# Performance work log

Hardware: AMD Instinct MI355X
Metric: run time of the kernel (lower is better)

The kernel has to match this reference:

```python
import jax, jax.numpy as jnp
import numpy as np

DIM = 1024
N_HEADS = 16
HEAD_DIM = DIM // N_HEADS
BATCH = 2
SEQ = 2048


def rotate_half(x):
    x1, x2 = jnp.split(x, 2, axis=-1)
    return jnp.concatenate((-x2, x1), axis=-1)


def rope_cos_sin(seq_len, head_dim, dtype=jnp.float32):
    inv_freq = 1.0 / (10000.0 ** (jnp.arange(0, head_dim, 2, dtype=jnp.float32) / head_dim))
    t = jnp.arange(seq_len, dtype=jnp.float32)
    freqs = jnp.einsum('i,j->ij', t, inv_freq)          # [S, hd/2]
    emb = jnp.concatenate((freqs, freqs), axis=-1)       # [S, hd]
    return emb.astype(dtype)[None, :, None, :]           # [1, S, 1, hd] (cos/sin applied below)


def setup_inputs() -> dict:
    key = jax.random.key(0)
    k_x, k_q, k_k, k_v, k_o = jax.random.split(key, 5)
    scale = 1.0 / np.sqrt(DIM)
    x = jax.random.normal(k_x, (BATCH, SEQ, DIM), dtype=jnp.float32)
    Wq = jax.random.normal(k_q, (DIM, DIM), dtype=jnp.float32) * scale
    Wk = jax.random.normal(k_k, (DIM, DIM), dtype=jnp.float32) * scale
    Wv = jax.random.normal(k_v, (DIM, DIM), dtype=jnp.float32) * scale
    Wo = jax.random.normal(k_o, (DIM, DIM), dtype=jnp.float32) * scale
    # causal mask: scores masked where mask == 0
    mask = jnp.tril(jnp.ones((SEQ, SEQ), dtype=jnp.int32))[None, None, :, :]
    return {"x": x, "Wq": Wq, "Wk": Wk, "Wv": Wv, "Wo": Wo, "mask": mask}


def reference(x, Wq, Wk, Wv, Wo, mask):
    B, S, _ = x.shape
    # torch nn.Linear: y = x @ W.T
    q = (x @ Wq.T).reshape(B, S, N_HEADS, HEAD_DIM)
    k = (x @ Wk.T).reshape(B, S, N_HEADS, HEAD_DIM)
    v = (x @ Wv.T).reshape(B, S, N_HEADS, HEAD_DIM)
    ang = rope_cos_sin(S, HEAD_DIM, x.dtype)
    cos, sin = jnp.cos(ang), jnp.sin(ang)
    q = q * cos + rotate_half(q) * sin
    k = k * cos + rotate_half(k) * sin
    # [B, H, S, hd]
    q = q.transpose(0, 2, 1, 3)
    k = k.transpose(0, 2, 1, 3)
    v = v.transpose(0, 2, 1, 3)
    scores = jnp.einsum('bhqd,bhkd->bhqk', q, k) / np.sqrt(HEAD_DIM)
    scores = jnp.where(mask == 0, jnp.asarray(-1e9, scores.dtype), scores)
    attn = jax.nn.softmax(scores, axis=-1)
    out = jnp.einsum('bhqk,bhkd->bhqd', attn, v)
    out = out.transpose(0, 2, 1, 3).reshape(B, S, DIM)
    return out @ Wo.T
```

## Files before the change

kernel.cpp:

```cpp
#include <hip/hip_runtime.h>
#include <stdint.h>

typedef unsigned short u16;
typedef __bf16 bf16x8 __attribute__((ext_vector_type(8)));
typedef __bf16 bf16x4 __attribute__((ext_vector_type(4)));
typedef float f32x4 __attribute__((ext_vector_type(4)));

#define N_B 2
#define N_S 2048
#define N_D 1024
#define N_H 16
#define HD 64

#if __has_builtin(__builtin_amdgcn_exp2f)
#define EXP2F(x) __builtin_amdgcn_exp2f(x)
#else
#define EXP2F(x) exp2f(x)
#endif

__device__ __forceinline__ u16 f2bf(float f) {
  union { float f; uint32_t u; } v; v.f = f;
  uint32_t u = v.u + 0x7fffu + ((v.u >> 16) & 1u);
  return (u16)(u >> 16);
}

__device__ __forceinline__ void gload16(const u16* g, u16* lds) {
  __builtin_amdgcn_global_load_lds(
      (const __attribute__((address_space(1))) unsigned int*)g,
      (__attribute__((address_space(3))) unsigned int*)lds, 16, 0, 0);
}

__global__ __launch_bounds__(256) void prep_kernel(
    const float* __restrict__ x, const float* __restrict__ Wq,
    const float* __restrict__ Wk, const float* __restrict__ Wv,
    const float* __restrict__ Wo,
    u16* __restrict__ xb, u16* __restrict__ wqb, u16* __restrict__ wkb,
    u16* __restrict__ wvb, u16* __restrict__ wob,
    float* __restrict__ cosT, float* __restrict__ sinT)
{
  const int NX = N_B * N_S * N_D;
  const int NW = N_D * N_D;
  int bid = blockIdx.x;
  if (bid < 8192) {
    int i = (bid * 256 + threadIdx.x) * 4;
    const float* src; u16* dst; int off;
    if (i < NX) { src = x; dst = xb; off = i; }
    else {
      int j = i - NX;
      int w = j >> 20;
      off = j & (NW - 1);
      src = (w == 0) ? Wq : (w == 1) ? Wk : (w == 2) ? Wv : Wo;
      dst = (w == 0) ? wqb : (w == 1) ? wkb : (w == 2) ? wvb : wob;
    }
    float4 v = *(const float4*)(src + off);
    ushort4 o;
    o.x = f2bf(v.x); o.y = f2bf(v.y); o.z = f2bf(v.z); o.w = f2bf(v.w);
    *(ushort4*)(dst + off) = o;
  } else {
    int t = (bid - 8192) * 256 + threadIdx.x;
    int s = t >> 5, i = t & 31;
    float inv = expf(-(float)i * 0.28782313662425574f);
    float a = (float)s * inv;
    float sn, cs;
    sincosf(a, &sn, &cs);
    cosT[t] = cs;
    sinT[t] = sn;
  }
}

__global__ __launch_bounds__(256, 5) void proj_kernel(
    const u16* __restrict__ x, const u16* __restrict__ Wq,
    const u16* __restrict__ Wk, const u16* __restrict__ Wv,
    u16* __restrict__ Qb, u16* __restrict__ Kb, u16* __restrict__ Vtb,
    const float* __restrict__ cosT, const float* __restrict__ sinT)
{
  const int mode = blockIdx.z;
  const u16* Wm = (mode == 0) ? Wq : (mode == 1) ? Wk : Wv;
  const int bx = blockIdx.x, by = blockIdx.y;
  const int tid = threadIdx.x;
  const int wave = tid >> 6, lane = tid & 63;
  const int c = lane & 15, quad = lane >> 4;

  __shared__ __align__(16) u16 As[128 * 64];
  __shared__ __align__(16) u16 Bs[64 * 64];

  const f32x4 zero = {0.f, 0.f, 0.f, 0.f};
  f32x4 acc[2][4];
#pragma unroll
  for (int i = 0; i < 2; ++i)
#pragma unroll
    for (int j = 0; j < 4; ++j) acc[i][j] = zero;

  for (int kt = 0; kt < 16; ++kt) {
    const int k0 = kt * 64;
    __syncthreads();
#pragma unroll
    for (int t = 0; t < 4; ++t) {
      int p = t * 256 + tid;
      int m = p >> 3, sl = p & 7;
      int kq = sl ^ (m & 7);
      gload16(x + (size_t)(by * 128 + m) * N_D + k0 + kq * 8, &As[(t * 256 + wave * 64) * 8]);
    }
#pragma unroll
    for (int t = 0; t < 2; ++t) {
      int p = t * 256 + tid;
      int m = p >> 3, sl = p & 7;
      int kq = sl ^ (m & 7);
      gload16(Wm + (size_t)(bx * 64 + m) * N_D + k0 + kq * 8, &Bs[(t * 256 + wave * 64) * 8]);
    }
    __syncthreads();
#pragma unroll
    for (int ks = 0; ks < 2; ++ks) {
      bf16x8 av[2], bv[4];
      int kq = ks * 4 + quad;
#pragma unroll
      for (int i = 0; i < 2; ++i) {
        int m = wave * 32 + i * 16 + c;
        av[i] = *(const bf16x8*)&As[(m * 8 + (kq ^ (m & 7))) * 8];
      }
#pragma unroll
      for (int j = 0; j < 4; ++j) {
        int n = j * 16 + c;
        bv[j] = *(const bf16x8*)&Bs[(n * 8 + (kq ^ (n & 7))) * 8];
      }
#pragma unroll
      for (int i = 0; i < 2; ++i)
#pragma unroll
        for (int j = 0; j < 4; ++j)
          acc[i][j] = __builtin_amdgcn_mfma_f32_16x16x32_bf16(av[i], bv[j], acc[i][j], 0, 0, 0);
    }
  }

  const int h = bx;
  if (mode < 2) {
    u16* Out = (mode == 0) ? Qb : Kb;
#pragma unroll
    for (int i = 0; i < 2; ++i) {
#pragma unroll
      for (int r = 0; r < 4; ++r) {
        int row = by * 128 + wave * 32 + i * 16 + quad * 4 + r;
        int b = row >> 11, s = row & 2047;
        float cs0 = cosT[s * 32 + c],      sn0 = sinT[s * 32 + c];
        float cs1 = cosT[s * 32 + 16 + c], sn1 = sinT[s * 32 + 16 + c];
        size_t base = ((size_t)(b * N_H + h) * N_S + s) * HD;
#pragma unroll
        for (int j = 0; j < 4; ++j) {
          float v = acc[i][j][r];
          float p = acc[i][j ^ 2][r];
          float cs = (j & 1) ? cs1 : cs0;
          float sn = (j & 1) ? sn1 : sn0;
          float res = (j < 2) ? (v * cs - p * sn) : (v * cs + p * sn);
          Out[base + j * 16 + c] = f2bf(res);
        }
      }
    }
  } else {
#pragma unroll
    for (int i = 0; i < 2; ++i) {
      int srow = by * 128 + wave * 32 + i * 16 + quad * 4;
      int b = srow >> 11, sb = srow & 2047;
#pragma unroll
      for (int j = 0; j < 4; ++j) {
        int d = j * 16 + c;
        ushort4 pk;
        pk.x = f2bf(acc[i][j][0]);
        pk.y = f2bf(acc[i][j][1]);
        pk.z = f2bf(acc[i][j][2]);
        pk.w = f2bf(acc[i][j][3]);
        *(ushort4*)&Vtb[((size_t)(b * N_H + h) * HD + d) * N_S + sb] = pk;
      }
    }
  }
}

__global__ __launch_bounds__(64, 2) void attn_kernel(
    const u16* __restrict__ Qb, const u16* __restrict__ Kb,
    const u16* __restrict__ Vtb, u16* __restrict__ Ab)
{
  const int lane = threadIdx.x;
  const int c = lane & 15, quad = lane >> 4;
  const int bx = blockIdx.x;
  const int xcd = bx & 7;
  const int idx = bx >> 3;
  const int t = 63 - (idx >> 2);
  const int bh = xcd + (idx & 3) * 8;
  const int q0 = t * 32;
  const int ktmax = t >> 1;
  const int maskch = t & 1;

  __shared__ __align__(16) u16 Ks[2][64 * 64];
  __shared__ __align__(16) u16 Ps[32 * 32];

  const u16* Qg = Qb + ((size_t)bh * N_S + q0) * HD;
  const u16* Kg = Kb + (size_t)bh * N_S * HD;
  const u16* Vg = Vtb + (size_t)bh * HD * N_S;

  bf16x8 qreg[2][2];
#pragma unroll
  for (int jQ = 0; jQ < 2; ++jQ)
#pragma unroll
    for (int ks = 0; ks < 2; ++ks)
      qreg[jQ][ks] = *(const bf16x8*)(Qg + (jQ * 16 + c) * HD + ks * 32 + quad * 8);

  const f32x4 zero = {0.f, 0.f, 0.f, 0.f};
  f32x4 acc_o[2][4];
#pragma unroll
  for (int mt = 0; mt < 2; ++mt)
#pragma unroll
    for (int nt = 0; nt < 4; ++nt) acc_o[mt][nt] = zero;
  float lrow[2] = {0.f, 0.f};

  const float CLOG = 0.18033688011112042f;
  const float FM = 16.0f;

#pragma unroll
  for (int i = 0; i < 8; ++i) {
    int ci = i * 64 + lane;
    int m = ci >> 3, sl = ci & 7;
    int kq = sl ^ (m & 7);
    gload16(Kg + (size_t)m * HD + kq * 8, &Ks[0][i * 512]);
  }
  asm volatile("" ::: "memory");
  bf16x8 vf[2][4];
#pragma unroll
  for (int ch = 0; ch < 2; ++ch)
#pragma unroll
    for (int nt = 0; nt < 4; ++nt)
      vf[ch][nt] = *(const bf16x8*)(Vg + (size_t)(nt * 16 + c) * N_S + ch * 32 + quad * 8);

  for (int kt = 0; kt <= ktmax; ++kt) {
    const u16* kb = &Ks[kt & 1][0];
    if (kt < ktmax) {
#pragma unroll
      for (int i = 0; i < 8; ++i) {
        int ci = i * 64 + lane;
        int m = ci >> 3, sl = ci & 7;
        int kq = sl ^ (m & 7);
        gload16(Kg + (size_t)((kt + 1) * 64 + m) * HD + kq * 8, &Ks[(kt + 1) & 1][i * 512]);
      }
      asm volatile("s_waitcnt vmcnt(16)" ::: "memory");
    } else {
      asm volatile("s_waitcnt vmcnt(8)" ::: "memory");
    }

    const bool diag = (kt == ktmax);
    const int nch = (diag && maskch == 0) ? 1 : 2;

#pragma unroll
    for (int ch = 0; ch < 2; ++ch) {
      if (ch < nch) {
        f32x4 acc_s[2][2];
#pragma unroll
        for (int iK = 0; iK < 2; ++iK)
#pragma unroll
          for (int jQ = 0; jQ < 2; ++jQ) acc_s[iK][jQ] = zero;
#pragma unroll
        for (int ks = 0; ks < 2; ++ks) {
          bf16x8 kf[2];
          int kq = ks * 4 + quad;
#pragma unroll
          for (int iK = 0; iK < 2; ++iK) {
            int m = ch * 32 + iK * 16 + c;
            kf[iK] = *(const bf16x8*)&kb[(m * 8 + (kq ^ (m & 7))) * 8];
          }
#pragma unroll
          for (int iK = 0; iK < 2; ++iK)
#pragma unroll
            for (int jQ = 0; jQ < 2; ++jQ)
              acc_s[iK][jQ] = __builtin_amdgcn_mfma_f32_16x16x32_bf16(
                  kf[iK], qreg[jQ][ks], acc_s[iK][jQ], 0, 0, 0);
        }

        const bool domask = diag && (ch == maskch);
#pragma unroll
        for (int iK = 0; iK < 2; ++iK)
#pragma unroll
          for (int jQ = 0; jQ < 2; ++jQ) {
            bf16x4 pb;
#pragma unroll
            for (int rr = 0; rr < 4; ++rr) {
              float arg = fmaf(acc_s[iK][jQ][rr], CLOG, -FM);
              if (domask) {
                int dsk = iK * 16 + quad * 4 + rr;
                int dq = jQ * 16 + c;
                if (dsk > dq) arg = -3.0e38f;
              }
              float p = EXP2F(arg);
              lrow[jQ] += p;
              pb[rr] = (__bf16)p;
            }
            int q = jQ * 16 + c;
            int slot = (iK * 2 + (quad >> 1)) ^ (q & 3);
            *(bf16x4*)&Ps[q * 32 + slot * 8 + (quad & 1) * 4] = pb;
          }

        bf16x8 pf[2];
#pragma unroll
        for (int mt = 0; mt < 2; ++mt) {
          int q = mt * 16 + c;
          pf[mt] = *(const bf16x8*)&Ps[q * 32 + ((quad ^ (q & 3)) * 8)];
        }
#pragma unroll
        for (int mt = 0; mt < 2; ++mt)
#pragma unroll
          for (int nt = 0; nt < 4; ++nt)
            acc_o[mt][nt] = __builtin_amdgcn_mfma_f32_16x16x32_bf16(
                pf[mt], vf[ch][nt], acc_o[mt][nt], 0, 0, 0);
      }
    }

    if (kt < ktmax) {
#pragma unroll
      for (int ch = 0; ch < 2; ++ch)
#pragma unroll
        for (int nt = 0; nt < 4; ++nt)
          vf[ch][nt] = *(const bf16x8*)(Vg + (size_t)(nt * 16 + c) * N_S
                                        + (kt + 1) * 64 + ch * 32 + quad * 8);
    }
  }

#pragma unroll
  for (int jQ = 0; jQ < 2; ++jQ) {
    float l = lrow[jQ];
    l += __shfl_xor(l, 16, 64);
    l += __shfl_xor(l, 32, 64);
    lrow[jQ] = 1.0f / l;
  }
  const int b = bh >> 4, h = bh & 15;
#pragma unroll
  for (int mt = 0; mt < 2; ++mt) {
#pragma unroll
    for (int rr = 0; rr < 4; ++rr) {
      float inv = __shfl(lrow[mt], quad * 4 + rr, 64);
      int q = q0 + mt * 16 + quad * 4 + rr;
#pragma unroll
      for (int nt = 0; nt < 4; ++nt) {
        Ab[((size_t)(b * N_S + q)) * N_D + h * HD + nt * 16 + c] =
            f2bf(acc_o[mt][nt][rr] * inv);
      }
    }
  }
}

__global__ __launch_bounds__(256) void out_gemm_kernel(
    const u16* __restrict__ A, const u16* __restrict__ Wo, float* __restrict__ out)
{
  const int bx = blockIdx.x, by = blockIdx.y;
  const int tid = threadIdx.x;
  const int wave = tid >> 6, lane = tid & 63;
  const int c = lane & 15, quad = lane >> 4;
  const int wm = wave & 1, wn = wave >> 1;

  __shared__ __align__(16) u16 As[64 * 64];
  __shared__ __align__(16) u16 Bs[64 * 64];

  const f32x4 zero = {0.f, 0.f, 0.f, 0.f};
  f32x4 acc[2][2];
#pragma unroll
  for (int i = 0; i < 2; ++i)
#pragma unroll
    for (int j = 0; j < 2; ++j) acc[i][j] = zero;

  for (int kt = 0; kt < 16; ++kt) {
    const int k0 = kt * 64;
    __syncthreads();
#pragma unroll
    for (int t = 0; t < 2; ++t) {
      int p = t * 256 + tid;
      int m = p >> 3, sl = p & 7;
      int kq = sl ^ (m & 7);
      gload16(A + (size_t)(by * 64 + m) * N_D + k0 + kq * 8, &As[(t * 256 + wave * 64) * 8]);
    }
#pragma unroll
    for (int t = 0; t < 2; ++t) {
      int p = t * 256 + tid;
      int m = p >> 3, sl = p & 7;
      int kq = sl ^ (m & 7);
      gload16(Wo + (size_t)(bx * 64 + m) * N_D + k0 + kq * 8, &Bs[(t * 256 + wave * 64) * 8]);
    }
    __syncthreads();
#pragma unroll
    for (int ks = 0; ks < 2; ++ks) {
      bf16x8 av[2], bv[2];
      int kq = ks * 4 + quad;
#pragma unroll
      for (int i = 0; i < 2; ++i) {
        int m = wm * 32 + i * 16 + c;
        av[i] = *(const bf16x8*)&As[(m * 8 + (kq ^ (m & 7))) * 8];
      }
#pragma unroll
      for (int j = 0; j < 2; ++j) {
        int n = wn * 32 + j * 16 + c;
        bv[j] = *(const bf16x8*)&Bs[(n * 8 + (kq ^ (n & 7))) * 8];
      }
#pragma unroll
      for (int i = 0; i < 2; ++i)
#pragma unroll
        for (int j = 0; j < 2; ++j)
          acc[i][j] = __builtin_amdgcn_mfma_f32_16x16x32_bf16(av[i], bv[j], acc[i][j], 0, 0, 0);
    }
  }

#pragma unroll
  for (int i = 0; i < 2; ++i)
#pragma unroll
    for (int r = 0; r < 4; ++r) {
      int row = by * 64 + wm * 32 + i * 16 + quad * 4 + r;
#pragma unroll
      for (int j = 0; j < 2; ++j) {
        int col = bx * 64 + wn * 32 + j * 16 + c;
        out[(size_t)row * N_D + col] = acc[i][j][r];
      }
    }
}

extern "C" void kernel_launch(void* const* d_in, const int* in_sizes, int n_in,
                              void* d_out, int out_size, void* d_ws, size_t ws_size,
                              hipStream_t stream) {
  const float* x  = (const float*)d_in[0];
  const float* Wq = (const float*)d_in[1];
  const float* Wk = (const float*)d_in[2];
  const float* Wv = (const float*)d_in[3];
  const float* Wo = (const float*)d_in[4];
  float* out = (float*)d_out;
  char* ws = (char*)d_ws;
  u16* xb   = (u16*)(ws);
  u16* Wqb  = (u16*)(ws + ( 8u << 20));
  u16* Wkb  = (u16*)(ws + (10u << 20));
  u16* Wvb  = (u16*)(ws + (12u << 20));
  u16* Wob  = (u16*)(ws + (14u << 20));
  u16* Qb   = (u16*)(ws + (16u << 20));
  u16* Kb   = (u16*)(ws + (24u << 20));
  u16* Vtb  = (u16*)(ws + (32u << 20));
  u16* Ab   = (u16*)(ws + (40u << 20));
  float* cosT = (float*)(ws + (48u << 20));
  float* sinT = (float*)(ws + (48u << 20) + (1u << 20));

  prep_kernel<<<8448, 256, 0, stream>>>(x, Wq, Wk, Wv, Wo,
                                        xb, Wqb, Wkb, Wvb, Wob, cosT, sinT);
  proj_kernel<<<dim3(16, 32, 3), 256, 0, stream>>>(xb, Wqb, Wkb, Wvb, Qb, Kb, Vtb, cosT, sinT);
  attn_kernel<<<2048, 64, 0, stream>>>(Qb, Kb, Vtb, Ab);
  out_gemm_kernel<<<dim3(16, 64), 256, 0, stream>>>(Ab, Wob, out);
}
```

Baseline: 206.0 us.

## Split attention key range across two waves per block and merge partial outputs

The attention kernel now runs two waves per block, and each wave handles half of the causal key tiles for the same 32-query tile, using its own K double buffer and P scratch in shared memory. Wave 1 writes its partial output accumulator and row sums to shared memory. After a barrier, wave 0 adds them to its own and normalises. The softmax uses a fixed max offset, so the partial sums combine directly. This is meant to cut the per-block serial latency of long causal rows and raise the number of active waves. The cost is doubled shared-memory use per block, a sync and a merge step, and an idle wave 1 during the final store.

```diff
diff --git a/kernel.cpp b/kernel.cpp
--- a/kernel.cpp
+++ b/kernel.cpp
@@ -173,11 +173,13 @@
   }
 }
 
-__global__ __launch_bounds__(64, 2) void attn_kernel(
+__global__ __launch_bounds__(128, 2) void attn_kernel(
     const u16* __restrict__ Qb, const u16* __restrict__ Kb,
     const u16* __restrict__ Vtb, u16* __restrict__ Ab)
 {
-  const int lane = threadIdx.x;
+  const int tid = threadIdx.x;
+  const int wave = tid >> 6;
+  const int lane = tid & 63;
   const int c = lane & 15, quad = lane >> 4;
   const int bx = blockIdx.x;
   const int xcd = bx & 7;
@@ -185,15 +187,20 @@
   const int t = 63 - (idx >> 2);
   const int bh = xcd + (idx & 3) * 8;
   const int q0 = t * 32;
-  const int ktmax = t >> 1;
+  const int nk = (t >> 1) + 1;
+  const int nk0 = (nk + 1) >> 1;
+  const int kb0 = wave ? nk0 : 0;
+  const int ke = wave ? nk : nk0;
   const int maskch = t & 1;
 
-  __shared__ __align__(16) u16 Ks[2][64 * 64];
-  __shared__ __align__(16) u16 Ps[32 * 32];
+  __shared__ __align__(16) u16 Ks[2][2][64 * 64];
+  __shared__ __align__(16) u16 Ps[2][32 * 32];
 
   const u16* Qg = Qb + ((size_t)bh * N_S + q0) * HD;
   const u16* Kg = Kb + (size_t)bh * N_S * HD;
   const u16* Vg = Vtb + (size_t)bh * HD * N_S;
+  u16* Psw = &Ps[wave][0];
+  u16* Ksw = &Ks[wave][0][0];
 
   bf16x8 qreg[2][2];
 #pragma unroll
@@ -213,37 +220,43 @@
   const float CLOG = 0.18033688011112042f;
   const float FM = 16.0f;
 
-#pragma unroll
-  for (int i = 0; i < 8; ++i) {
-    int ci = i * 64 + lane;
-    int m = ci >> 3, sl = ci & 7;
-    int kq = sl ^ (m & 7);
-    gload16(Kg + (size_t)m * HD + kq * 8, &Ks[0][i * 512]);
-  }
-  asm volatile("" ::: "memory");
   bf16x8 vf[2][4];
-#pragma unroll
-  for (int ch = 0; ch < 2; ++ch)
-#pragma unroll
-    for (int nt = 0; nt < 4; ++nt)
-      vf[ch][nt] = *(const bf16x8*)(Vg + (size_t)(nt * 16 + c) * N_S + ch * 32 + quad * 8);
-
-  for (int kt = 0; kt <= ktmax; ++kt) {
-    const u16* kb = &Ks[kt & 1][0];
-    if (kt < ktmax) {
+
+  if (kb0 < ke) {
+#pragma unroll
+    for (int i = 0; i < 8; ++i) {
+      int ci = i * 64 + lane;
+      int m = ci >> 3, sl = ci & 7;
+      int kq = sl ^ (m & 7);
+      gload16(Kg + (size_t)(kb0 * 64 + m) * HD + kq * 8,
+              &Ksw[(kb0 & 1) * 4096 + i * 512]);
+    }
+    asm volatile("" ::: "memory");
+#pragma unroll
+    for (int ch = 0; ch < 2; ++ch)
+#pragma unroll
+      for (int nt = 0; nt < 4; ++nt)
+        vf[ch][nt] = *(const bf16x8*)(Vg + (size_t)(nt * 16 + c) * N_S
+                                      + kb0 * 64 + ch * 32 + quad * 8);
+  }
+
+  for (int kt = kb0; kt < ke; ++kt) {
+    const u16* kbp = &Ksw[(kt & 1) * 4096];
+    if (kt + 1 < ke) {
 #pragma unroll
       for (int i = 0; i < 8; ++i) {
         int ci = i * 64 + lane;
         int m = ci >> 3, sl = ci & 7;
         int kq = sl ^ (m & 7);
-        gload16(Kg + (size_t)((kt + 1) * 64 + m) * HD + kq * 8, &Ks[(kt + 1) & 1][i * 512]);
+        gload16(Kg + (size_t)((kt + 1) * 64 + m) * HD + kq * 8,
+                &Ksw[((kt + 1) & 1) * 4096 + i * 512]);
       }
       asm volatile("s_waitcnt vmcnt(16)" ::: "memory");
     } else {
       asm volatile("s_waitcnt vmcnt(8)" ::: "memory");
     }
 
-    const bool diag = (kt == ktmax);
+    const bool diag = (kt == nk - 1);
     const int nch = (diag && maskch == 0) ? 1 : 2;
 
 #pragma unroll
@@ -261,7 +274,7 @@
 #pragma unroll
           for (int iK = 0; iK < 2; ++iK) {
             int m = ch * 32 + iK * 16 + c;
-            kf[iK] = *(const bf16x8*)&kb[(m * 8 + (kq ^ (m & 7))) * 8];
+            kf[iK] = *(const bf16x8*)&kbp[(m * 8 + (kq ^ (m & 7))) * 8];
           }
 #pragma unroll
           for (int iK = 0; iK < 2; ++iK)
@@ -291,14 +304,14 @@
             }
             int q = jQ * 16 + c;
             int slot = (iK * 2 + (quad >> 1)) ^ (q & 3);
-            *(bf16x4*)&Ps[q * 32 + slot * 8 + (quad & 1) * 4] = pb;
+            *(bf16x4*)&Psw[q * 32 + slot * 8 + (quad & 1) * 4] = pb;
           }
 
         bf16x8 pf[2];
 #pragma unroll
         for (int mt = 0; mt < 2; ++mt) {
           int q = mt * 16 + c;
-          pf[mt] = *(const bf16x8*)&Ps[q * 32 + ((quad ^ (q & 3)) * 8)];
+          pf[mt] = *(const bf16x8*)&Psw[q * 32 + ((quad ^ (q & 3)) * 8)];
         }
 #pragma unroll
         for (int mt = 0; mt < 2; ++mt)
@@ -309,7 +322,7 @@
       }
     }
 
-    if (kt < ktmax) {
+    if (kt + 1 < ke) {
 #pragma unroll
       for (int ch = 0; ch < 2; ++ch)
 #pragma unroll
@@ -324,19 +337,40 @@
     float l = lrow[jQ];
     l += __shfl_xor(l, 16, 64);
     l += __shfl_xor(l, 32, 64);
-    lrow[jQ] = 1.0f / l;
-  }
-  const int b = bh >> 4, h = bh & 15;
-#pragma unroll
-  for (int mt = 0; mt < 2; ++mt) {
-#pragma unroll
-    for (int rr = 0; rr < 4; ++rr) {
-      float inv = __shfl(lrow[mt], quad * 4 + rr, 64);
-      int q = q0 + mt * 16 + quad * 4 + rr;
-#pragma unroll
-      for (int nt = 0; nt < 4; ++nt) {
-        Ab[((size_t)(b * N_S + q)) * N_D + h * HD + nt * 16 + c] =
-            f2bf(acc_o[mt][nt][rr] * inv);
+    lrow[jQ] = l;
+  }
+
+  float* Osh = (float*)&Ks[1][0][0];
+  float* Lsh = Osh + 32 * 65;
+  if (wave == 1) {
+#pragma unroll
+    for (int mt = 0; mt < 2; ++mt)
+#pragma unroll
+      for (int nt = 0; nt < 4; ++nt)
+#pragma unroll
+        for (int rr = 0; rr < 4; ++rr)
+          Osh[(mt * 16 + quad * 4 + rr) * 65 + nt * 16 + c] = acc_o[mt][nt][rr];
+    if (quad == 0) { Lsh[c] = lrow[0]; Lsh[16 + c] = lrow[1]; }
+  }
+  __syncthreads();
+  if (wave == 0) {
+    float inv[2];
+#pragma unroll
+    for (int jQ = 0; jQ < 2; ++jQ)
+      inv[jQ] = 1.0f / (lrow[jQ] + Lsh[jQ * 16 + c]);
+    const int b = bh >> 4, h = bh & 15;
+#pragma unroll
+    for (int mt = 0; mt < 2; ++mt) {
+#pragma unroll
+      for (int rr = 0; rr < 4; ++rr) {
+        float iv = __shfl(inv[mt], quad * 4 + rr, 64);
+        int lr = mt * 16 + quad * 4 + rr;
+        int q = q0 + lr;
+#pragma unroll
+        for (int nt = 0; nt < 4; ++nt) {
+          float val = (acc_o[mt][nt][rr] + Osh[lr * 65 + nt * 16 + c]) * iv;
+          Ab[((size_t)(b * N_S + q)) * N_D + h * HD + nt * 16 + c] = f2bf(val);
+        }
       }
     }
   }
@@ -439,6 +473,6 @@
   prep_kernel<<<8448, 256, 0, stream>>>(x, Wq, Wk, Wv, Wo,
                                         xb, Wqb, Wkb, Wvb, Wob, cosT, sinT);
   proj_kernel<<<dim3(16, 32, 3), 256, 0, stream>>>(xb, Wqb, Wkb, Wvb, Qb, Kb, Vtb, cosT, sinT);
-  attn_kernel<<<2048, 64, 0, stream>>>(Qb, Kb, Vtb, Ab);
+  attn_kernel<<<2048, 128, 0, stream>>>(Qb, Kb, Vtb, Ab);
   out_gemm_kernel<<<dim3(16, 64), 256, 0, stream>>>(Ab, Wob, out);
 }
```

After: 200.1 us. -2.9%, faster.
